# Performance work log

Measured on AMD Instinct MI355X. Metric: run time of the kernel, lower is better.

The kernel has to match this reference:

```python
import jax, jax.numpy as jnp
import numpy as np

N, D, H, HD, R, K, TM = 32768, 128, 2, 64, 2, 32, 2
E_EDGES, M_MOTIFS, NG = 262144, 131072, 32
EPS = 1e-5
BETA_MAX = 5.0
GRAD_CLIP = 1.0
STATE_CLIP = 10.0
DAMPING = 1.0

def _isp(x):
    # inverse softplus of init values (params stored pre-softplus)
    return float(np.log(np.expm1(x)))

LAM2_RAW, LAM3_RAW, LAMM_RAW = _isp(1.0), _isp(0.5), _isp(1.0)
B2_RAW, B3_RAW, BM_RAW = _isp(1.0), _isp(1.0), _isp(1.0)


def layernorm(x, g, b):
    mu = x.mean(-1, keepdims=True)
    v = ((x - mu) ** 2).mean(-1, keepdims=True)
    return g * (x - mu) * jax.lax.rsqrt(v + EPS) + b


def seg_lse(s, seg, n, beta):
    # tempered logsumexp over segments: (1/beta) log sum_j exp(beta*s_j); s:[items,H] -> [n,H]
    sb = beta * s
    m = jax.ops.segment_max(sb, seg, num_segments=n)
    m = jnp.where(jnp.isfinite(m), m, 0.0)
    z = jax.ops.segment_sum(jnp.exp(sb - m[seg]), seg, num_segments=n)
    return jnp.where(z > 0, (m + jnp.log(jnp.maximum(z, 1e-30))) / beta, 0.0)


def energy(X, a_2, ln_gamma, ln_beta, W_Q2, W_K2, W_Q3, W_K3, T_tau, W_Qm, W_Km, B_mem,
           c_2, u_2, c_3, u_3, v_3, t_tau, batch):
    sp = jax.nn.softplus
    lam2, lam3, lamm = sp(LAM2_RAW), sp(LAM3_RAW), sp(LAMM_RAW)
    b2 = jnp.minimum(sp(B2_RAW), BETA_MAX)
    b3 = jnp.minimum(sp(B3_RAW), BETA_MAX)
    bm = jnp.minimum(sp(BM_RAW), BETA_MAX)
    G = layernorm(X, ln_gamma, ln_beta)
    # pairwise Q2/K2 term over edges (c_2 <- u_2) with learned per-edge bias a_2
    Q2 = jnp.einsum('nd,hzd->nhz', G, W_Q2)  # [N,H,HD]
    K2 = jnp.einsum('nd,hzd->nhz', G, W_K2)
    s2 = jnp.einsum('ehz,ehz->eh', Q2[c_2], K2[u_2]) / np.sqrt(HD) + a_2  # [E,H]
    e_pair = -lam2 * seg_lse(s2, c_2, N, b2).sum(-1)  # [N]
    # rank-R bilinear motif term over (c_3,u_3,v_3) with type embedding T_tau
    Q3 = jnp.einsum('nd,hzd->nhz', G, W_Q3).reshape(N, H, R, HD)
    K3 = jnp.einsum('nd,hzd->nhz', G, W_K3).reshape(N, H, R, HD)
    qk = jnp.einsum('mhrz,mhrz->mhr', Q3[c_3], K3[u_3])
    tv = jnp.einsum('mhrz,mhrz->mhr', T_tau[t_tau], K3[v_3])
    s3 = (qk * tv).sum(-1) / HD  # [M,H]
    e_motif = -lam3 * seg_lse(s3, c_3, N, b3).sum(-1)
    # K-slot memory term
    Qm = jnp.einsum('nd,hzd->nhz', G, W_Qm)
    Km = jnp.einsum('kd,hzd->hkz', B_mem, W_Km)
    sm = jnp.einsum('nhz,hkz->nhk', Qm, Km) / np.sqrt(HD)
    e_mem = -(lamm / bm) * jax.nn.logsumexp(bm * sm, axis=-1).sum(-1)
    e_node = 0.5 * (X * X).sum(-1) + e_pair + e_motif + e_mem
    return jax.ops.segment_sum(e_node, batch, num_segments=NG)  # per-graph energy [NG]


def setup_inputs() -> dict:
    key = jax.random.key(0)
    ks = jax.random.split(key, 16)
    inp = {}
    inp['X'] = jax.random.normal(ks[0], (N, D), jnp.float32)
    inp['c_2'] = jax.random.randint(ks[1], (E_EDGES,), 0, N)
    inp['u_2'] = jax.random.randint(ks[2], (E_EDGES,), 0, N)
    inp['c_3'] = jax.random.randint(ks[3], (M_MOTIFS,), 0, N)
    inp['u_3'] = jax.random.randint(ks[4], (M_MOTIFS,), 0, N)
    inp['v_3'] = jax.random.randint(ks[5], (M_MOTIFS,), 0, N)
    inp['t_tau'] = jax.random.randint(ks[6], (M_MOTIFS,), 0, TM)
    inp['batch'] = jnp.sort(jax.random.randint(ks[7], (N,), 0, NG))
    inp['a_2'] = 0.1 * jax.random.normal(ks[8], (E_EDGES, H), jnp.float32)
    inp['step_size'] = jnp.full((1,), 0.1, jnp.float32)
    inp['ln_gamma'] = jnp.ones((D,), jnp.float32)
    inp['ln_beta'] = jnp.zeros((D,), jnp.float32)
    s = 1.0 / np.sqrt(D)
    inp['W_Q2'] = s * jax.random.normal(ks[9], (H, HD, D), jnp.float32)
    inp['W_K2'] = s * jax.random.normal(ks[10], (H, HD, D), jnp.float32)
    inp['W_Q3'] = 0.5 * s * jax.random.normal(ks[11], (H, R * HD, D), jnp.float32)
    inp['W_K3'] = 0.5 * s * jax.random.normal(ks[12], (H, R * HD, D), jnp.float32)
    inp['T_tau'] = 0.02 * jax.random.normal(ks[13], (TM, H, R, HD), jnp.float32)
    inp['W_Qm'] = 0.5 * s * jax.random.normal(ks[14], (H, HD, D), jnp.float32)
    inp['W_Km'] = 0.5 * s * jax.random.normal(ks[15], (H, HD, D), jnp.float32)
    inp['B_mem'] = s * jax.random.normal(jax.random.fold_in(key, 99), (K, D), jnp.float32)
    return inp


def reference(X, c_2, u_2, c_3, u_3, v_3, t_tau, batch, a_2, step_size,
              ln_gamma, ln_beta, W_Q2, W_K2, W_Q3, W_K3, T_tau, W_Qm, W_Km, B_mem):
    Eg, vjp = jax.vjp(
        lambda Xv: energy(Xv, a_2, ln_gamma, ln_beta, W_Q2, W_K2, W_Q3, W_K3, T_tau,
                          W_Qm, W_Km, B_mem, c_2, u_2, c_3, u_3, v_3, t_tau, batch), X)
    gX, = vjp(jnp.ones_like(Eg))
    gnorm = jnp.linalg.norm(gX, axis=-1, keepdims=True)
    gX = gX * (GRAD_CLIP / jnp.maximum(gnorm, GRAD_CLIP))
    X_next = X - step_size[0] * DAMPING * gX
    snorm = jnp.linalg.norm(X_next, axis=-1, keepdims=True)
    X_next = X_next * (STATE_CLIP / jnp.maximum(snorm, STATE_CLIP))
    return X_next, Eg
```

## Files before the change

kernel.cpp:

```cpp
#include <hip/hip_runtime.h>
#include <hip/hip_bf16.h>
#include <math.h>

typedef __hip_bfloat16 bf16;
typedef short bf16x8 __attribute__((ext_vector_type(8)));
typedef float f32x4 __attribute__((ext_vector_type(4)));

#define N_NODES 32768
#define D_DIM 128
#define E_EDG 262144
#define M_MOT 131072
#define NG_G 32
#define F_TOT 832

__device__ __forceinline__ float wsum64(float v){
#pragma unroll
  for (int o = 32; o > 0; o >>= 1) v += __shfl_xor(v, o, 64);
  return v;
}
__device__ __forceinline__ float hsum32(float v){
#pragma unroll
  for (int o = 16; o > 0; o >>= 1) v += __shfl_xor(v, o, 64);
  return v;
}
__device__ __forceinline__ float hmax32(float v){
#pragma unroll
  for (int o = 16; o > 0; o >>= 1) v = fmaxf(v, __shfl_xor(v, o, 64));
  return v;
}
__device__ __forceinline__ float hsum8(float v){
#pragma unroll
  for (int o = 4; o > 0; o >>= 1) v += __shfl_xor(v, o, 64);
  return v;
}
__device__ __forceinline__ float bflo(unsigned u){ return __uint_as_float(u << 16); }
__device__ __forceinline__ float bfhi(unsigned u){ return __uint_as_float(u & 0xffff0000u); }
__device__ __forceinline__ unsigned packbf(float x, float y){
  bf16 a = __float2bfloat16(x), b = __float2bfloat16(y);
  unsigned short ua = *(unsigned short*)&a, ub = *(unsigned short*)&b;
  return (unsigned)ua | ((unsigned)ub << 16);
}
__device__ __forceinline__ void unpk8(uint4 p, float* f){
  f[0] = bflo(p.x); f[1] = bfhi(p.x); f[2] = bflo(p.y); f[3] = bfhi(p.y);
  f[4] = bflo(p.z); f[5] = bfhi(p.z); f[6] = bflo(p.w); f[7] = bfhi(p.w);
}

__global__ __launch_bounds__(256) void k_phaseA(
    const int* c2, const int* u2, const int* c3, const int* u3, const int* v3,
    const float* wq2, const float* wk2, const float* wq3, const float* wk3,
    const float* wqm, const float* wkm, const float* bmem, const float* Ttau,
    int* cnt, float* Wcat, bf16* Ttb, float* Mprod){
  __shared__ float KmL[64];
  int b = blockIdx.x, t = threadIdx.x;
  if (b < 1024){
    int i = b * 256 + t;
    atomicAdd(&cnt[c2[i]], 1);
    atomicAdd(&cnt[N_NODES + u2[i]], 1);
    if (i < M_MOT){
      atomicAdd(&cnt[2 * N_NODES + c3[i]], 1);
      atomicAdd(&cnt[3 * N_NODES + u3[i]], 1);
      atomicAdd(&cnt[4 * N_NODES + v3[i]], 1);
    }
  } else if (b < 1440){
    int idx = (b - 1024) * 256 + t;
    if (idx < 768 * D_DIM){
      int f = idx / D_DIM, d = idx - f * D_DIM;
      const float* src; int fr;
      if      (f < 128){ src = wq2; fr = f; }
      else if (f < 256){ src = wk2; fr = f - 128; }
      else if (f < 512){ src = wq3; fr = f - 256; }
      else             { src = wk3; fr = f - 512; }
      Wcat[f * D_DIM + d] = src[fr * D_DIM + d];
    } else {
      int j = idx - 768 * D_DIM;
      Ttb[j] = __float2bfloat16(Ttau[j]);
    }
  } else {
    int hk = b - 1440;
    int h = hk >> 5, k = hk & 31;
    if (t < 64){
      const float* wrow = wkm + (size_t)(h * 64 + t) * D_DIM;
      const float* brow = bmem + k * D_DIM;
      float acc = 0.f;
      for (int d = 0; d < D_DIM; d++) acc += wrow[d] * brow[d];
      KmL[t] = acc;
    }
    __syncthreads();
    if (t < 128){
      const float* w = wqm + (size_t)(h * 64) * 128 + t;
      float acc = 0.f;
      for (int z = 0; z < 64; z++) acc += w[z * 128] * KmL[z];
      Mprod[t * 64 + hk] = acc;
    }
  }
}

__global__ __launch_bounds__(1024) void k_phaseB(
    int* cntcur, int* off,
    const float* X, const float* gamma, const float* beta,
    bf16* Gb, float* mu, float* rstd, float* e_node,
    const float* Wcat, const float* Mprod, bf16* wfF, bf16* wfB){
  __shared__ int sd[1024];
  int b = blockIdx.x, t = threadIdx.x;
  if (b < 5){
    int a = b;
    int* c = cntcur + a * N_NODES;
    int* o = off + a * (N_NODES + 1);
    int loc[32];
    int sum = 0;
#pragma unroll
    for (int j = 0; j < 32; j++){ loc[j] = sum; sum += c[t * 32 + j]; }
    sd[t] = sum;
    __syncthreads();
    for (int s = 1; s < 1024; s <<= 1){
      int v = (t >= s) ? sd[t - s] : 0;
      __syncthreads();
      sd[t] += v;
      __syncthreads();
    }
    int excl = sd[t] - sum;
#pragma unroll
    for (int j = 0; j < 32; j++){
      int val = excl + loc[j];
      o[t * 32 + j] = val;
      c[t * 32 + j] = val;
    }
    if (t == 1023) o[N_NODES] = sd[1023];
  } else if (b < 2053){
    int wv = t >> 6, l = t & 63;
    int n = (b - 5) * 16 + wv;
    float2 x2 = ((const float2*)(X + (size_t)n * 128))[l];
    float sumx = wsum64(x2.x + x2.y);
    float sumxx = wsum64(x2.x * x2.x + x2.y * x2.y);
    float m = sumx * (1.0f / 128.0f);
    float var = sumxx * (1.0f / 128.0f) - m * m;
    float rs = rsqrtf(var + 1e-5f);
    float2 gg = ((const float2*)gamma)[l];
    float2 bb = ((const float2*)beta)[l];
    ((unsigned*)(Gb + (size_t)n * 128))[l] =
        packbf(gg.x * (x2.x - m) * rs + bb.x, gg.y * (x2.y - m) * rs + bb.y);
    if (l == 0){ mu[n] = m; rstd[n] = rs; e_node[n] = 0.5f * sumxx; }
  } else {
    int idx = (b - 2053) * 1024 + t;
    int j = idx & 7, lane = (idx >> 3) & 63, tt = idx >> 9;
    {
      int tn = tt >> 2, kt = tt & 3;
      int f = tn * 16 + (lane & 15), d = kt * 32 + (lane >> 4) * 8 + j;
      float v = (f < 768) ? Wcat[f * 128 + d] : 0.125f * Mprod[d * 64 + (f - 768)];
      wfF[idx] = __float2bfloat16(v);
    }
    {
      int td = tt / 26, tf = tt - td * 26;
      int f = tf * 32 + (lane >> 4) * 8 + j, d = td * 16 + (lane & 15);
      float v = (f < 768) ? Wcat[f * 128 + d] : -0.125f * Mprod[d * 64 + (f - 768)];
      wfB[idx] = __float2bfloat16(v);
    }
  }
}

__global__ __launch_bounds__(256) void k_phaseC(
    const bf16* Gb, const bf16* wfF, bf16* P,
    const int* c2, const int* u2, const int* c3, const int* u3, const int* v3,
    const int* tt, const float* a2, int* cur,
    uint2* lec, uint2* leu, uint2* lmc, uint2* lmu, uint2* lmv){
  int b = blockIdx.x;
  int g = b / 15, r = b - g * 15;
  if (r < 13){
    __shared__ unsigned shP[64 * 36];
    int f = g * 13 + r;
    int bx = f & 511, by = f >> 9;
    int wave = threadIdx.x >> 6, lane = threadIdx.x & 63;
    int m0 = bx * 64 + wave * 16;
    int tn0 = by * 4;
    int rw = lane & 15, quad = lane >> 4;
    const bf16* aptr = Gb + (size_t)(m0 + rw) * 128 + quad * 8;
    bf16x8 a[4];
#pragma unroll
    for (int kt = 0; kt < 4; kt++) a[kt] = *(const bf16x8*)(aptr + kt * 32);
    f32x4 acc[4];
#pragma unroll
    for (int i = 0; i < 4; i++) acc[i] = (f32x4){0.f, 0.f, 0.f, 0.f};
#pragma unroll
    for (int nf = 0; nf < 4; nf++){
      int tn = tn0 + nf;
#pragma unroll
      for (int kt = 0; kt < 4; kt++){
        bf16x8 bb = *(const bf16x8*)(wfF + (((size_t)tn * 4 + kt) * 64 + lane) * 8);
        acc[nf] = __builtin_amdgcn_mfma_f32_16x16x32_bf16(bb, a[kt], acc[nf], 0, 0, 0);
      }
    }
    int lrow = wave * 16 + rw;
#pragma unroll
    for (int nf = 0; nf < 4; nf++){
      unsigned lo = packbf(acc[nf][0], acc[nf][1]);
      unsigned hi = packbf(acc[nf][2], acc[nf][3]);
      *(uint2*)&shP[lrow * 36 + nf * 8 + quad * 2] = make_uint2(lo, hi);
    }
    __syncthreads();
    int t = threadIdx.x;
    int orow = t >> 2, s = t & 3;
    uint4 v0 = *(const uint4*)&shP[orow * 36 + s * 4];
    uint4 v1 = *(const uint4*)&shP[orow * 36 + 16 + s * 4];
    uint4* prow = (uint4*)(P + (size_t)(bx * 64 + orow) * F_TOT) + tn0 * 2 + s;
    prow[0] = v0;
    prow[4] = v1;
  } else {
    int i = (g * 2 + (r - 13)) * 256 + threadIdx.x;
    {
      int c = c2[i], u = u2[i];
      int posc = atomicAdd(&cur[c], 1);
      float2 av = *(const float2*)(a2 + (size_t)i * 2);
      lec[posc] = make_uint2((unsigned)u, packbf(av.x, av.y));
      int posu = atomicAdd(&cur[N_NODES + u], 1);
      leu[posu] = make_uint2((unsigned)c, (unsigned)posc);
    }
    if (i < M_MOT){
      int c = c3[i], u = u3[i], v = v3[i], t = tt[i];
      int posc = atomicAdd(&cur[2 * N_NODES + c], 1);
      lmc[posc] = make_uint2((unsigned)(u | (v << 16)), (unsigned)t);
      int posu = atomicAdd(&cur[3 * N_NODES + u], 1);
      lmu[posu] = make_uint2((unsigned)c, (unsigned)posc);
      int posv = atomicAdd(&cur[4 * N_NODES + v], 1);
      lmv[posv] = make_uint2((unsigned)(c | (t << 16)), (unsigned)posc);
    }
  }
}

__global__ __launch_bounds__(256) void k_fused_c(const bf16* P, const uint2* lec, const uint2* lmc,
                   const bf16* Ttb, const int* off_ec, const int* off_mc,
                   float* s2, float* rz2, float* s3, float* qkb, float* tvb, float* rz3,
                   bf16* dP, float* e_pair, float* e_mot, float* e_mem){
  int b = blockIdx.x;
  int type = b % 3, grp = b / 3;
  int wave = threadIdx.x >> 6, z = threadIdx.x & 63;
  int n = grp * 4 + wave;
  int l = z & 31, lh = z >> 5;

  if (type == 0){
    int q = z >> 4, l16 = z & 15, hg = l16 >> 3;
    int beg = off_ec[n], end = off_ec[n + 1];
    uint4 qp = ((const uint4*)(P + (size_t)n * F_TOT))[l16];
    float qv[8]; unpk8(qp, qv);
    float acc[8] = {0,0,0,0,0,0,0,0};
    float zz = 0.f;
    int iters = (end - beg + 3) >> 2;
    for (int it = 0; it < iters; it++){
      int idx = beg + 4 * it + q;
      bool valid = idx < end;
      int idc = valid ? idx : end - 1;
      uint2 pl = lec[idc];
      uint4 kp = ((const uint4*)(P + (size_t)pl.x * F_TOT + 128))[l16];
      float kv[8]; unpk8(kp, kv);
      float d = 0.f;
#pragma unroll
      for (int j = 0; j < 8; j++) d += qv[j] * kv[j];
      float s = hsum8(d) * 0.125f + (hg ? bfhi(pl.y) : bflo(pl.y));
      if (valid && (l16 & 7) == 0) s2[2 * idx + hg] = s;
      float ex = valid ? expf(s) : 0.f;
#pragma unroll
      for (int j = 0; j < 8; j++) acc[j] += ex * kv[j];
      zz += ex;
    }
#pragma unroll
    for (int j = 0; j < 8; j++){
      acc[j] += __shfl_xor(acc[j], 16, 64);
      acc[j] += __shfl_xor(acc[j], 32, 64);
    }
    zz += __shfl_xor(zz, 16, 64);
    zz += __shfl_xor(zz, 32, 64);
    float rz = (zz > 0.f) ? 1.0f / zz : 0.f;
    float coef = -0.125f * rz;
    if (z < 16){
      uint4 o;
      o.x = packbf(coef * acc[0], coef * acc[1]);
      o.y = packbf(coef * acc[2], coef * acc[3]);
      o.z = packbf(coef * acc[4], coef * acc[5]);
      o.w = packbf(coef * acc[6], coef * acc[7]);
      ((uint4*)(dP + (size_t)n * F_TOT))[l16] = o;
      if ((l16 & 7) == 0) rz2[n * 2 + hg] = rz;
    }
    float eterm = (zz > 0.f) ? -logf(zz) : 0.f;
    float eo = __shfl(eterm, 8, 64);
    if (z == 0) e_pair[n] = eterm + eo;
  } else if (type == 1){
    int g = l >> 3, hg = g >> 1;
    int beg = off_mc[n], end = off_mc[n + 1];
    uint4 qp = ((const uint4*)(P + (size_t)n * F_TOT + 256))[l];
    float qv[8]; unpk8(qp, qv);
    float acc[8] = {0,0,0,0,0,0,0,0};
    float zz = 0.f;
    int iters = (end - beg + 1) >> 1;
    for (int it = 0; it < iters; it++){
      int idx = beg + 2 * it + lh;
      bool valid = idx < end;
      int idc = valid ? idx : end - 1;
      uint2 pl = lmc[idc];
      int u = pl.x & 0xffff, v = pl.x >> 16, t = pl.y;
      uint4 kup = ((const uint4*)(P + (size_t)u * F_TOT + 512))[l];
      uint4 kvp = ((const uint4*)(P + (size_t)v * F_TOT + 512))[l];
      uint4 tp  = ((const uint4*)(Ttb + (size_t)t * 256))[l];
      float k[8], vv[8], pt[8];
      unpk8(kup, k); unpk8(kvp, vv); unpk8(tp, pt);
      float dq = 0.f, dt = 0.f;
#pragma unroll
      for (int j = 0; j < 8; j++){ dq += qv[j] * k[j]; dt += pt[j] * vv[j]; }
      float qk = hsum8(dq);
      float tv = hsum8(dt);
      if (valid && (l & 7) == 0){ qkb[(size_t)4 * idx + g] = qk; tvb[(size_t)4 * idx + g] = tv; }
      float w = qk * tv;
      float s = (w + __shfl_xor(w, 8, 64)) * (1.0f / 64.0f);
      if (valid && (l & 15) == 0) s3[2 * idx + hg] = s;
      float ex = valid ? expf(s) : 0.f;
      float et = ex * tv;
#pragma unroll
      for (int j = 0; j < 8; j++) acc[j] += et * k[j];
      zz += ex;
    }
#pragma unroll
    for (int j = 0; j < 8; j++) acc[j] += __shfl_xor(acc[j], 32, 64);
    zz += __shfl_xor(zz, 32, 64);
    float rz = (zz > 0.f) ? 1.0f / zz : 0.f;
    float coef = (-0.5f / 64.0f) * rz;
    if (z < 32){
      uint4 o;
      o.x = packbf(coef * acc[0], coef * acc[1]);
      o.y = packbf(coef * acc[2], coef * acc[3]);
      o.z = packbf(coef * acc[4], coef * acc[5]);
      o.w = packbf(coef * acc[6], coef * acc[7]);
      ((uint4*)(dP + (size_t)n * F_TOT + 256))[l] = o;
      if ((l & 15) == 0) rz3[n * 2 + hg] = rz;
    }
    float eterm = (zz > 0.f) ? -0.5f * logf(zz) : 0.f;
    float eo = __shfl(eterm, 16, 64);
    if (z == 0) e_mot[n] = eterm + eo;
  } else {
    unsigned short us = ((const unsigned short*)(P + (size_t)n * F_TOT + 768))[z];
    float s = __uint_as_float((unsigned)us << 16);
    float mx = hmax32(s);
    float ex = expf(s - mx);
    float se = hsum32(ex);
    float p = ex / se;
    bf16 pb = __float2bfloat16(p);
    ((unsigned short*)(dP + (size_t)n * F_TOT + 768))[z] = *(unsigned short*)&pb;
    float eterm = -(mx + logf(se));
    float eo = __shfl(eterm, z ^ 32, 64);
    if (z == 0) e_mem[n] = eterm + eo;
  }
}

__global__ __launch_bounds__(256) void k_phaseE(const bf16* P, const uint2* leu,
                    const uint2* lmu, const uint2* lmv, const bf16* Ttb,
                    const float* s2, const float* rz2, const float* s3, const float* rz3,
                    const float* qkb, const float* tvb,
                    const int* off_eu, const int* off_mu, const int* off_mv, bf16* dP,
                    const float* e_node, const float* e_pair, const float* e_mot,
                    const float* e_mem, const int* batch, float* Eg){
  __shared__ float eg[NG_G];
  int b = blockIdx.x;
  if (b < 128){
    int t = threadIdx.x;
    if (t < NG_G) eg[t] = 0.f;
    __syncthreads();
    int n = b * 256 + t;
    float e = e_node[n] + e_pair[n] + e_mot[n] + e_mem[n];
    atomicAdd(&eg[batch[n]], e);
    __syncthreads();
    if (t < NG_G) atomicAdd(&Eg[t], eg[t]);
    return;
  }
  int b2 = b - 128;
  int type = b2 & 1, grp = b2 >> 1;
  int wave = threadIdx.x >> 6, z = threadIdx.x & 63;
  int n = grp * 4 + wave;
  int l = z & 31, lh = z >> 5;

  if (type == 0){
    int q = z >> 4, l16 = z & 15, hg = l16 >> 3;
    int beg = off_eu[n], end = off_eu[n + 1];
    float acc[8] = {0,0,0,0,0,0,0,0};
    int iters = (end - beg + 3) >> 2;
    for (int it = 0; it < iters; it++){
      int idx = beg + 4 * it + q;
      bool valid = idx < end;
      int idc = valid ? idx : end - 1;
      uint2 pl = leu[idc];
      uint4 qp = ((const uint4*)(P + (size_t)pl.x * F_TOT))[l16];
      float qv[8]; unpk8(qp, qv);
      float p = valid ? expf(s2[2 * pl.y + hg]) * rz2[pl.x * 2 + hg] : 0.f;
#pragma unroll
      for (int j = 0; j < 8; j++) acc[j] += p * qv[j];
    }
#pragma unroll
    for (int j = 0; j < 8; j++){
      acc[j] += __shfl_xor(acc[j], 16, 64);
      acc[j] += __shfl_xor(acc[j], 32, 64);
    }
    if (z < 16){
      uint4 o;
      o.x = packbf(-0.125f * acc[0], -0.125f * acc[1]);
      o.y = packbf(-0.125f * acc[2], -0.125f * acc[3]);
      o.z = packbf(-0.125f * acc[4], -0.125f * acc[5]);
      o.w = packbf(-0.125f * acc[6], -0.125f * acc[7]);
      ((uint4*)(dP + (size_t)n * F_TOT + 128))[l16] = o;
    }
  } else {
    int g = l >> 3, hg = g >> 1;
    float acc[8] = {0,0,0,0,0,0,0,0};
    {
      int beg = off_mu[n], end = off_mu[n + 1];
      int iters = (end - beg + 1) >> 1;
      for (int it = 0; it < iters; it++){
        int idx = beg + 2 * it + lh;
        bool valid = idx < end;
        int idc = valid ? idx : end - 1;
        uint2 pl = lmu[idc];
        unsigned c = pl.x, posc = pl.y;
        uint4 qp = ((const uint4*)(P + (size_t)c * F_TOT + 256))[l];
        float qv[8]; unpk8(qp, qv);
        float w = valid ? expf(s3[2 * posc + hg]) * rz3[c * 2 + hg] * tvb[(size_t)4 * posc + g] : 0.f;
#pragma unroll
        for (int j = 0; j < 8; j++) acc[j] += w * qv[j];
      }
    }
    {
      int beg = off_mv[n], end = off_mv[n + 1];
      int iters = (end - beg + 1) >> 1;
      for (int it = 0; it < iters; it++){
        int idx = beg + 2 * it + lh;
        bool valid = idx < end;
        int idc = valid ? idx : end - 1;
        uint2 pl = lmv[idc];
        unsigned c = pl.x & 0xffff, t = pl.x >> 16, posc = pl.y;
        uint4 tp = ((const uint4*)(Ttb + (size_t)t * 256))[l];
        float pt[8]; unpk8(tp, pt);
        float w = valid ? expf(s3[2 * posc + hg]) * rz3[c * 2 + hg] * qkb[(size_t)4 * posc + g] : 0.f;
#pragma unroll
        for (int j = 0; j < 8; j++) acc[j] += w * pt[j];
      }
    }
#pragma unroll
    for (int j = 0; j < 8; j++) acc[j] += __shfl_xor(acc[j], 32, 64);
    const float cst = -0.5f / 64.0f;
    if (z < 32){
      uint4 o;
      o.x = packbf(cst * acc[0], cst * acc[1]);
      o.y = packbf(cst * acc[2], cst * acc[3]);
      o.z = packbf(cst * acc[4], cst * acc[5]);
      o.w = packbf(cst * acc[6], cst * acc[7]);
      ((uint4*)(dP + (size_t)n * F_TOT + 512))[l] = o;
    }
  }
}

__global__ __launch_bounds__(256) void k_bwd_mfma(const bf16* dP, const bf16* wfB, float* dG){
  int wave = threadIdx.x >> 6, lane = threadIdx.x & 63;
  int m0 = blockIdx.x * 64 + wave * 16;
  int rw = lane & 15, quad = lane >> 4;
  const bf16* aptr = dP + (size_t)(m0 + rw) * F_TOT + quad * 8;
  f32x4 acc[8];
#pragma unroll
  for (int i = 0; i < 8; i++) acc[i] = (f32x4){0.f, 0.f, 0.f, 0.f};
  for (int kt = 0; kt < 26; kt++){
    bf16x8 a = *(const bf16x8*)(aptr + kt * 32);
#pragma unroll
    for (int td = 0; td < 8; td++){
      bf16x8 b = *(const bf16x8*)(wfB + (((size_t)td * 26 + kt) * 64 + lane) * 8);
      acc[td] = __builtin_amdgcn_mfma_f32_16x16x32_bf16(a, b, acc[td], 0, 0, 0);
    }
  }
#pragma unroll
  for (int td = 0; td < 8; td++){
    int col = td * 16 + rw;
#pragma unroll
    for (int r = 0; r < 4; r++){
      int row = m0 + quad * 4 + r;
      dG[(size_t)row * 128 + col] = acc[td][r];
    }
  }
}

__global__ __launch_bounds__(256) void k_finalize(const float* X, const float* dG, const float* gamma,
                    const float* mu, const float* rstd, const float* step_p,
                    const float* Eg, float* out){
  int wave = threadIdx.x >> 6, l = threadIdx.x & 63;
  int n = blockIdx.x * 4 + wave;
  float2 x2 = ((const float2*)(X + (size_t)n * 128))[l];
  float2 dg2 = ((const float2*)(dG + (size_t)n * 128))[l];
  float2 gg = ((const float2*)gamma)[l];
  float rs = rstd[n], m = mu[n];
  float xh0 = (x2.x - m) * rs, xh1 = (x2.y - m) * rs;
  float dxh0 = dg2.x * gg.x, dxh1 = dg2.y * gg.y;
  float s1 = wsum64(dxh0 + dxh1);
  float s2v = wsum64(dxh0 * xh0 + dxh1 * xh1);
  float g0 = x2.x + rs * (dxh0 - s1 * (1.0f / 128) - xh0 * (s2v * (1.0f / 128)));
  float g1 = x2.y + rs * (dxh1 - s1 * (1.0f / 128) - xh1 * (s2v * (1.0f / 128)));
  float gn = sqrtf(wsum64(g0 * g0 + g1 * g1));
  float gc = 1.0f / fmaxf(gn, 1.0f);
  g0 *= gc; g1 *= gc;
  float step = step_p[0];
  float xn0 = x2.x - step * g0, xn1 = x2.y - step * g1;
  float sn = sqrtf(wsum64(xn0 * xn0 + xn1 * xn1));
  float sc = 10.0f / fmaxf(sn, 10.0f);
  ((float2*)(out + (size_t)n * 128))[l] = make_float2(xn0 * sc, xn1 * sc);
  if (blockIdx.x == 0 && threadIdx.x < NG_G)
    out[(size_t)N_NODES * 128 + threadIdx.x] = Eg[threadIdx.x];
}

extern "C" void kernel_launch(void* const* d_in, const int* in_sizes, int n_in,
                              void* d_out, int out_size, void* d_ws, size_t ws_size,
                              hipStream_t stream) {
  const float* X     = (const float*)d_in[0];
  const int*  c_2    = (const int*) d_in[1];
  const int*  u_2    = (const int*) d_in[2];
  const int*  c_3    = (const int*) d_in[3];
  const int*  u_3    = (const int*) d_in[4];
  const int*  v_3    = (const int*) d_in[5];
  const int*  t_tau  = (const int*) d_in[6];
  const int*  batch  = (const int*) d_in[7];
  const float* a_2   = (const float*)d_in[8];
  const float* step_s= (const float*)d_in[9];
  const float* ln_g  = (const float*)d_in[10];
  const float* ln_b  = (const float*)d_in[11];
  const float* W_Q2  = (const float*)d_in[12];
  const float* W_K2  = (const float*)d_in[13];
  const float* W_Q3  = (const float*)d_in[14];
  const float* W_K3  = (const float*)d_in[15];
  const float* T_tau = (const float*)d_in[16];
  const float* W_Qm  = (const float*)d_in[17];
  const float* W_Km  = (const float*)d_in[18];
  const float* B_mem = (const float*)d_in[19];
  float* out = (float*)d_out;

  char* wb = (char*)d_ws;
  float* Wcat   = (float*)wb; wb += 768 * D_DIM * 4;
  float* Mprod  = (float*)wb; wb += 8192 * 4;
  float* mu     = (float*)wb; wb += N_NODES * 4;
  float* rstd   = (float*)wb; wb += N_NODES * 4;
  float* s2     = (float*)wb; wb += (size_t)E_EDG * 2 * 4;
  float* rz2    = (float*)wb; wb += N_NODES * 2 * 4;
  float* s3     = (float*)wb; wb += (size_t)M_MOT * 2 * 4;
  float* qkb    = (float*)wb; wb += (size_t)M_MOT * 4 * 4;
  float* tvb    = (float*)wb; wb += (size_t)M_MOT * 4 * 4;
  float* rz3    = (float*)wb; wb += N_NODES * 2 * 4;
  float* e_node = (float*)wb; wb += N_NODES * 4;
  float* e_pair = (float*)wb; wb += N_NODES * 4;
  float* e_mot  = (float*)wb; wb += N_NODES * 4;
  float* e_mem  = (float*)wb; wb += N_NODES * 4;
  float* Eg     = (float*)wb; wb += NG_G * 4;
  float* dG     = (float*)wb; wb += (size_t)N_NODES * D_DIM * 4;
  bf16* Gb      = (bf16*)wb;  wb += (size_t)N_NODES * D_DIM * 2;
  bf16* P       = (bf16*)wb;  wb += (size_t)N_NODES * F_TOT * 2;
  bf16* dP      = (bf16*)wb;  wb += (size_t)N_NODES * F_TOT * 2;
  bf16* wfF     = (bf16*)wb;  wb += 106496 * 2;
  bf16* wfB     = (bf16*)wb;  wb += 106496 * 2;
  bf16* Ttb     = (bf16*)wb;  wb += 8192 * 2;
  int* cntcur   = (int*)wb;   wb += 5 * N_NODES * 4;
  int* off      = (int*)wb;   wb += 5 * (N_NODES + 1) * 4;
  wb = (char*)(((size_t)wb + 15) & ~(size_t)15);
  uint2* lec    = (uint2*)wb; wb += (size_t)E_EDG * 8;
  uint2* leu    = (uint2*)wb; wb += (size_t)E_EDG * 8;
  uint2* lmc    = (uint2*)wb; wb += (size_t)M_MOT * 8;
  uint2* lmu    = (uint2*)wb; wb += (size_t)M_MOT * 8;
  uint2* lmv    = (uint2*)wb; wb += (size_t)M_MOT * 8;

  const int* off_ec = off;
  const int* off_eu = off + (N_NODES + 1);
  const int* off_mc = off + 2 * (N_NODES + 1);
  const int* off_mu = off + 3 * (N_NODES + 1);
  const int* off_mv = off + 4 * (N_NODES + 1);

  hipMemsetAsync(cntcur, 0, 5 * N_NODES * sizeof(int), stream);
  hipMemsetAsync(Eg, 0, NG_G * sizeof(float), stream);
  hipLaunchKernelGGL(k_phaseA, dim3(1504), dim3(256), 0, stream,
                     c_2, u_2, c_3, u_3, v_3, W_Q2, W_K2, W_Q3, W_K3,
                     W_Qm, W_Km, B_mem, T_tau, cntcur, Wcat, Ttb, Mprod);
  hipLaunchKernelGGL(k_phaseB, dim3(2157), dim3(1024), 0, stream,
                     cntcur, off, X, ln_g, ln_b, Gb, mu, rstd, e_node,
                     Wcat, Mprod, wfF, wfB);
  hipLaunchKernelGGL(k_phaseC, dim3(7680), dim3(256), 0, stream,
                     Gb, wfF, P, c_2, u_2, c_3, u_3, v_3, t_tau, a_2, cntcur,
                     lec, leu, lmc, lmu, lmv);
  hipLaunchKernelGGL(k_fused_c, dim3(3 * (N_NODES / 4)), dim3(256), 0, stream,
                     P, lec, lmc, Ttb, off_ec, off_mc,
                     s2, rz2, s3, qkb, tvb, rz3, dP, e_pair, e_mot, e_mem);
  hipLaunchKernelGGL(k_phaseE, dim3(128 + 2 * (N_NODES / 4)), dim3(256), 0, stream,
                     P, leu, lmu, lmv, Ttb, s2, rz2, s3, rz3, qkb, tvb,
                     off_eu, off_mu, off_mv, dP,
                     e_node, e_pair, e_mot, e_mem, batch, Eg);
  hipLaunchKernelGGL(k_bwd_mfma, dim3(N_NODES / 64), dim3(256), 0, stream, dP, wfB, dG);
  hipLaunchKernelGGL(k_finalize, dim3(N_NODES / 4), dim3(256), 0, stream,
                     X, dG, ln_g, mu, rstd, step_s, Eg, out);
}
```

Baseline: 380.7 us.

## Partition CSR-build atomics by node residue to keep counters XCD-local

The counting and scatter phases are split so each block only does atomics for nodes whose low three bits match its residue, which follows the block's position modulo 8. Counters are stored in a permuted layout (pidx) so each residue class is contiguous. The intent is to keep atomic traffic within one L2/XCD slice instead of spreading contended atomics across all of them. CSR entries now hold the original edge or motif index instead of a packed bias and slot position. The a_2 bias is therefore read in the gather kernel, and per-edge scores are indexed by original id. The cost is reading the index arrays eight times and more scattered score writes.

```diff
diff --git a/kernel.cpp b/kernel.cpp
--- a/kernel.cpp
+++ b/kernel.cpp
@@ -12,6 +12,8 @@
 #define M_MOT 131072
 #define NG_G 32
 #define F_TOT 832
+
+__device__ __forceinline__ int pidx(int n){ return ((n & 7) << 12) | (n >> 3); }
 
 __device__ __forceinline__ float wsum64(float v){
 #pragma unroll
@@ -52,17 +54,21 @@
     int* cnt, float* Wcat, bf16* Ttb, float* Mprod){
   __shared__ float KmL[64];
   int b = blockIdx.x, t = threadIdx.x;
-  if (b < 1024){
-    int i = b * 256 + t;
-    atomicAdd(&cnt[c2[i]], 1);
-    atomicAdd(&cnt[N_NODES + u2[i]], 1);
+  if (b < 8192){
+    int range = b >> 3;
+    int res = b & 7;
+    int i = range * 256 + t;
+    int c = c2[i], u = u2[i];
+    if ((c & 7) == res) atomicAdd(&cnt[pidx(c)], 1);
+    if ((u & 7) == res) atomicAdd(&cnt[N_NODES + pidx(u)], 1);
     if (i < M_MOT){
-      atomicAdd(&cnt[2 * N_NODES + c3[i]], 1);
-      atomicAdd(&cnt[3 * N_NODES + u3[i]], 1);
-      atomicAdd(&cnt[4 * N_NODES + v3[i]], 1);
-    }
-  } else if (b < 1440){
-    int idx = (b - 1024) * 256 + t;
+      int cc = c3[i], uu = u3[i], vv = v3[i];
+      if ((cc & 7) == res) atomicAdd(&cnt[2 * N_NODES + pidx(cc)], 1);
+      if ((uu & 7) == res) atomicAdd(&cnt[3 * N_NODES + pidx(uu)], 1);
+      if ((vv & 7) == res) atomicAdd(&cnt[4 * N_NODES + pidx(vv)], 1);
+    }
+  } else if (b < 8608){
+    int idx = (b - 8192) * 256 + t;
     if (idx < 768 * D_DIM){
       int f = idx / D_DIM, d = idx - f * D_DIM;
       const float* src; int fr;
@@ -76,7 +82,7 @@
       Ttb[j] = __float2bfloat16(Ttau[j]);
     }
   } else {
-    int hk = b - 1440;
+    int hk = b - 8608;
     int h = hk >> 5, k = hk & 31;
     if (t < 64){
       const float* wrow = wkm + (size_t)(h * 64 + t) * D_DIM;
@@ -161,10 +167,10 @@
 __global__ __launch_bounds__(256) void k_phaseC(
     const bf16* Gb, const bf16* wfF, bf16* P,
     const int* c2, const int* u2, const int* c3, const int* u3, const int* v3,
-    const int* tt, const float* a2, int* cur,
+    const int* t3, int* cur,
     uint2* lec, uint2* leu, uint2* lmc, uint2* lmu, uint2* lmv){
   int b = blockIdx.x;
-  int g = b / 15, r = b - g * 15;
+  int g = b / 29, r = b - g * 29;
   if (r < 13){
     __shared__ unsigned shP[64 * 36];
     int f = g * 13 + r;
@@ -205,29 +211,41 @@
     prow[0] = v0;
     prow[4] = v1;
   } else {
-    int i = (g * 2 + (r - 13)) * 256 + threadIdx.x;
+    int j = g * 16 + (r - 13);
+    int range = j >> 3;
+    int res = b & 7;
+    int i = range * 256 + threadIdx.x;
     {
       int c = c2[i], u = u2[i];
-      int posc = atomicAdd(&cur[c], 1);
-      float2 av = *(const float2*)(a2 + (size_t)i * 2);
-      lec[posc] = make_uint2((unsigned)u, packbf(av.x, av.y));
-      int posu = atomicAdd(&cur[N_NODES + u], 1);
-      leu[posu] = make_uint2((unsigned)c, (unsigned)posc);
+      if ((c & 7) == res){
+        int pos = atomicAdd(&cur[pidx(c)], 1);
+        lec[pos] = make_uint2((unsigned)u, (unsigned)i);
+      }
+      if ((u & 7) == res){
+        int pos = atomicAdd(&cur[N_NODES + pidx(u)], 1);
+        leu[pos] = make_uint2((unsigned)c, (unsigned)i);
+      }
     }
     if (i < M_MOT){
-      int c = c3[i], u = u3[i], v = v3[i], t = tt[i];
-      int posc = atomicAdd(&cur[2 * N_NODES + c], 1);
-      lmc[posc] = make_uint2((unsigned)(u | (v << 16)), (unsigned)t);
-      int posu = atomicAdd(&cur[3 * N_NODES + u], 1);
-      lmu[posu] = make_uint2((unsigned)c, (unsigned)posc);
-      int posv = atomicAdd(&cur[4 * N_NODES + v], 1);
-      lmv[posv] = make_uint2((unsigned)(c | (t << 16)), (unsigned)posc);
+      int c = c3[i], u = u3[i], v = v3[i], mt = t3[i];
+      if ((c & 7) == res){
+        int pos = atomicAdd(&cur[2 * N_NODES + pidx(c)], 1);
+        lmc[pos] = make_uint2((unsigned)(u | (v << 16)), (unsigned)(mt | (i << 5)));
+      }
+      if ((u & 7) == res){
+        int pos = atomicAdd(&cur[3 * N_NODES + pidx(u)], 1);
+        lmu[pos] = make_uint2((unsigned)c, (unsigned)i);
+      }
+      if ((v & 7) == res){
+        int pos = atomicAdd(&cur[4 * N_NODES + pidx(v)], 1);
+        lmv[pos] = make_uint2((unsigned)(c | (mt << 16)), (unsigned)i);
+      }
     }
   }
 }
 
 __global__ __launch_bounds__(256) void k_fused_c(const bf16* P, const uint2* lec, const uint2* lmc,
-                   const bf16* Ttb, const int* off_ec, const int* off_mc,
+                   const bf16* Ttb, const float* a2, const int* off_ec, const int* off_mc,
                    float* s2, float* rz2, float* s3, float* qkb, float* tvb, float* rz3,
                    bf16* dP, float* e_pair, float* e_mot, float* e_mem){
   int b = blockIdx.x;
@@ -235,10 +253,11 @@
   int wave = threadIdx.x >> 6, z = threadIdx.x & 63;
   int n = grp * 4 + wave;
   int l = z & 31, lh = z >> 5;
+  int pn = pidx(n);
 
   if (type == 0){
     int q = z >> 4, l16 = z & 15, hg = l16 >> 3;
-    int beg = off_ec[n], end = off_ec[n + 1];
+    int beg = off_ec[pn], end = off_ec[pn + 1];
     uint4 qp = ((const uint4*)(P + (size_t)n * F_TOT))[l16];
     float qv[8]; unpk8(qp, qv);
     float acc[8] = {0,0,0,0,0,0,0,0};
@@ -249,13 +268,14 @@
       bool valid = idx < end;
       int idc = valid ? idx : end - 1;
       uint2 pl = lec[idc];
+      float2 av = *(const float2*)(a2 + (size_t)pl.y * 2);
       uint4 kp = ((const uint4*)(P + (size_t)pl.x * F_TOT + 128))[l16];
       float kv[8]; unpk8(kp, kv);
       float d = 0.f;
 #pragma unroll
       for (int j = 0; j < 8; j++) d += qv[j] * kv[j];
-      float s = hsum8(d) * 0.125f + (hg ? bfhi(pl.y) : bflo(pl.y));
-      if (valid && (l16 & 7) == 0) s2[2 * idx + hg] = s;
+      float s = hsum8(d) * 0.125f + (hg ? av.y : av.x);
+      if (valid && (l16 & 7) == 0) s2[2 * pl.y + hg] = s;
       float ex = valid ? expf(s) : 0.f;
 #pragma unroll
       for (int j = 0; j < 8; j++) acc[j] += ex * kv[j];
@@ -284,7 +304,7 @@
     if (z == 0) e_pair[n] = eterm + eo;
   } else if (type == 1){
     int g = l >> 3, hg = g >> 1;
-    int beg = off_mc[n], end = off_mc[n + 1];
+    int beg = off_mc[pn], end = off_mc[pn + 1];
     uint4 qp = ((const uint4*)(P + (size_t)n * F_TOT + 256))[l];
     float qv[8]; unpk8(qp, qv);
     float acc[8] = {0,0,0,0,0,0,0,0};
@@ -295,10 +315,11 @@
       bool valid = idx < end;
       int idc = valid ? idx : end - 1;
       uint2 pl = lmc[idc];
-      int u = pl.x & 0xffff, v = pl.x >> 16, t = pl.y;
+      int u = pl.x & 0xffff, v = pl.x >> 16;
+      int tix = pl.y & 31; unsigned m = pl.y >> 5;
       uint4 kup = ((const uint4*)(P + (size_t)u * F_TOT + 512))[l];
       uint4 kvp = ((const uint4*)(P + (size_t)v * F_TOT + 512))[l];
-      uint4 tp  = ((const uint4*)(Ttb + (size_t)t * 256))[l];
+      uint4 tp  = ((const uint4*)(Ttb + (size_t)tix * 256))[l];
       float k[8], vv[8], pt[8];
       unpk8(kup, k); unpk8(kvp, vv); unpk8(tp, pt);
       float dq = 0.f, dt = 0.f;
@@ -306,10 +327,10 @@
       for (int j = 0; j < 8; j++){ dq += qv[j] * k[j]; dt += pt[j] * vv[j]; }
       float qk = hsum8(dq);
       float tv = hsum8(dt);
-      if (valid && (l & 7) == 0){ qkb[(size_t)4 * idx + g] = qk; tvb[(size_t)4 * idx + g] = tv; }
+      if (valid && (l & 7) == 0){ qkb[(size_t)4 * m + g] = qk; tvb[(size_t)4 * m + g] = tv; }
       float w = qk * tv;
       float s = (w + __shfl_xor(w, 8, 64)) * (1.0f / 64.0f);
-      if (valid && (l & 15) == 0) s3[2 * idx + hg] = s;
+      if (valid && (l & 15) == 0) s3[2 * m + hg] = s;
       float ex = valid ? expf(s) : 0.f;
       float et = ex * tv;
 #pragma unroll
@@ -373,10 +394,11 @@
   int wave = threadIdx.x >> 6, z = threadIdx.x & 63;
   int n = grp * 4 + wave;
   int l = z & 31, lh = z >> 5;
+  int pn = pidx(n);
 
   if (type == 0){
     int q = z >> 4, l16 = z & 15, hg = l16 >> 3;
-    int beg = off_eu[n], end = off_eu[n + 1];
+    int beg = off_eu[pn], end = off_eu[pn + 1];
     float acc[8] = {0,0,0,0,0,0,0,0};
     int iters = (end - beg + 3) >> 2;
     for (int it = 0; it < iters; it++){
@@ -407,33 +429,33 @@
     int g = l >> 3, hg = g >> 1;
     float acc[8] = {0,0,0,0,0,0,0,0};
     {
-      int beg = off_mu[n], end = off_mu[n + 1];
+      int beg = off_mu[pn], end = off_mu[pn + 1];
       int iters = (end - beg + 1) >> 1;
       for (int it = 0; it < iters; it++){
         int idx = beg + 2 * it + lh;
         bool valid = idx < end;
         int idc = valid ? idx : end - 1;
         uint2 pl = lmu[idc];
-        unsigned c = pl.x, posc = pl.y;
+        unsigned c = pl.x, m = pl.y;
         uint4 qp = ((const uint4*)(P + (size_t)c * F_TOT + 256))[l];
         float qv[8]; unpk8(qp, qv);
-        float w = valid ? expf(s3[2 * posc + hg]) * rz3[c * 2 + hg] * tvb[(size_t)4 * posc + g] : 0.f;
+        float w = valid ? expf(s3[2 * m + hg]) * rz3[c * 2 + hg] * tvb[(size_t)4 * m + g] : 0.f;
 #pragma unroll
         for (int j = 0; j < 8; j++) acc[j] += w * qv[j];
       }
     }
     {
-      int beg = off_mv[n], end = off_mv[n + 1];
+      int beg = off_mv[pn], end = off_mv[pn + 1];
       int iters = (end - beg + 1) >> 1;
       for (int it = 0; it < iters; it++){
         int idx = beg + 2 * it + lh;
         bool valid = idx < end;
         int idc = valid ? idx : end - 1;
         uint2 pl = lmv[idc];
-        unsigned c = pl.x & 0xffff, t = pl.x >> 16, posc = pl.y;
-        uint4 tp = ((const uint4*)(Ttb + (size_t)t * 256))[l];
+        unsigned c = pl.x & 0xffff, tix = pl.x >> 16, m = pl.y;
+        uint4 tp = ((const uint4*)(Ttb + (size_t)tix * 256))[l];
         float pt[8]; unpk8(tp, pt);
-        float w = valid ? expf(s3[2 * posc + hg]) * rz3[c * 2 + hg] * qkb[(size_t)4 * posc + g] : 0.f;
+        float w = valid ? expf(s3[2 * m + hg]) * rz3[c * 2 + hg] * qkb[(size_t)4 * m + g] : 0.f;
 #pragma unroll
         for (int j = 0; j < 8; j++) acc[j] += w * pt[j];
       }
@@ -571,17 +593,17 @@
 
   hipMemsetAsync(cntcur, 0, 5 * N_NODES * sizeof(int), stream);
   hipMemsetAsync(Eg, 0, NG_G * sizeof(float), stream);
-  hipLaunchKernelGGL(k_phaseA, dim3(1504), dim3(256), 0, stream,
+  hipLaunchKernelGGL(k_phaseA, dim3(8672), dim3(256), 0, stream,
                      c_2, u_2, c_3, u_3, v_3, W_Q2, W_K2, W_Q3, W_K3,
                      W_Qm, W_Km, B_mem, T_tau, cntcur, Wcat, Ttb, Mprod);
   hipLaunchKernelGGL(k_phaseB, dim3(2157), dim3(1024), 0, stream,
                      cntcur, off, X, ln_g, ln_b, Gb, mu, rstd, e_node,
                      Wcat, Mprod, wfF, wfB);
-  hipLaunchKernelGGL(k_phaseC, dim3(7680), dim3(256), 0, stream,
-                     Gb, wfF, P, c_2, u_2, c_3, u_3, v_3, t_tau, a_2, cntcur,
+  hipLaunchKernelGGL(k_phaseC, dim3(512 * 29), dim3(256), 0, stream,
+                     Gb, wfF, P, c_2, u_2, c_3, u_3, v_3, t_tau, cntcur,
                      lec, leu, lmc, lmu, lmv);
   hipLaunchKernelGGL(k_fused_c, dim3(3 * (N_NODES / 4)), dim3(256), 0, stream,
-                     P, lec, lmc, Ttb, off_ec, off_mc,
+                     P, lec, lmc, Ttb, a_2, off_ec, off_mc,
                      s2, rz2, s3, qkb, tvb, rz3, dP, e_pair, e_mot, e_mem);
   hipLaunchKernelGGL(k_phaseE, dim3(128 + 2 * (N_NODES / 4)), dim3(256), 0, stream,
                      P, leu, lmu, lmv, Ttb, s2, rz2, s3, rz3, qkb, tvb,
```

After: 381.5 us. Within noise of the previous version (+0.2%).
